# Optimization experiments

Measured on AMD Instinct MI355X. Metric: run time of the kernel, lower is better.

Reference implementation:

```python
import jax, jax.numpy as jnp
import numpy as np
import math

S, B, H, NH = 2048, 2, 2048, 16
HN = H // NH  # 128, head dim


def _rope_cache(seq_len, hn):
    # inv_freqs over even indices, half_hn entries
    inv_freqs = 0.0001 ** (jnp.arange(0, hn, 2, dtype=jnp.float32) / hn)
    pos = jnp.arange(seq_len, dtype=jnp.float32)
    angles = pos[:, None] * inv_freqs  # [s, hn/2]
    return jnp.cos(angles), jnp.sin(angles)


def _apply_rope(x, cos, sin):
    # x: [s, b, np, hn]; cos/sin: [s, hn/2] broadcast over b, np
    half = x.shape[-1] // 2
    c = cos[:, None, None, :]
    s = sin[:, None, None, :]
    left, right = x[..., :half], x[..., half:]
    return jnp.concatenate((c * left - s * right, s * left + c * right), axis=-1)


def setup_inputs() -> dict:
    key = jax.random.key(0)
    k0, k1, k2 = jax.random.split(key, 3)
    hidden_states = jax.random.normal(k0, (S, B, H), dtype=jnp.float32)
    # causal additive mask, broadcast over batch and heads
    causal = jnp.tril(jnp.ones((S, S), dtype=bool))
    attention_mask = jnp.where(causal, 0.0, -1e9).astype(jnp.float32)[None, None]
    W_qkv = jax.random.normal(k1, (3 * H, H), dtype=jnp.float32) * 0.02
    b_qkv = jnp.zeros((3 * H,), dtype=jnp.float32)
    W_dense = jax.random.normal(k2, (H, H), dtype=jnp.float32) * 0.02
    b_dense = jnp.zeros((H,), dtype=jnp.float32)
    return {"hidden_states": hidden_states, "attention_mask": attention_mask,
            "W_qkv": W_qkv, "b_qkv": b_qkv, "W_dense": W_dense, "b_dense": b_dense}


def reference(hidden_states, attention_mask, W_qkv, b_qkv, W_dense, b_dense):
    s, b, h = hidden_states.shape
    # fused QKV projection: [s,b,3h] -> [s,b,np,3*hn] -> split per head
    mixed = hidden_states @ W_qkv.T + b_qkv
    mixed = mixed.reshape(s, b, NH, 3 * HN)
    q, k, v = jnp.split(mixed, 3, axis=-1)  # each [s,b,np,hn]
    cos, sin = _rope_cache(s, HN)
    q = _apply_rope(q, cos, sin)
    k = _apply_rope(k, cos, sin)
    norm_factor = math.sqrt(HN)  # coeff is None (scale_attn_by_inverse_layer_idx=False)
    scores = jnp.einsum('sbnh,tbnh->bnst', q, k) / norm_factor  # [b,np,sq,sk]
    scores = scores + attention_mask
    probs = jax.nn.softmax(scores, axis=-1)  # dropout p=0 in eval
    ctx = jnp.einsum('bnst,tbnh->sbnh', probs, v).reshape(s, b, h)
    return ctx @ W_dense.T + b_dense  # [s,b,h]
```

## Files before the change

### kernel.cpp

```cpp
#include <hip/hip_runtime.h>

#define SEQ   2048
#define BATCH 2
#define HID   2048
#define NHEAD 16
#define HDIM  128
#define MTOT  4096
#define KDIM  2048

typedef __attribute__((ext_vector_type(8))) short  bf16x8;
typedef __attribute__((ext_vector_type(4))) float  f32x4;
typedef __attribute__((ext_vector_type(4))) unsigned short u16x4;
typedef __attribute__((ext_vector_type(8))) unsigned short u16x8;

__device__ __forceinline__ unsigned short f2bf(float x) {
  unsigned u = __float_as_uint(x);
  u += 0x7fffu + ((u >> 16) & 1u);
  return (unsigned short)(u >> 16);
}

__device__ __forceinline__ float fexp2(float x) {
  float r;
  asm("v_exp_f32 %0, %1" : "=v"(r) : "v"(x));
  return r;
}

__device__ __forceinline__ void gl_lds16(const void* g, void* l) {
  __builtin_amdgcn_global_load_lds(
      (__attribute__((address_space(1))) void*)g,
      (__attribute__((address_space(3))) void*)l, 16, 0, 0);
}

__device__ __forceinline__ f32x4 mfma16(bf16x8 a, bf16x8 b, f32x4 c) {
  return __builtin_amdgcn_mfma_f32_16x16x32_bf16(a, b, c, 0, 0, 0);
}

__global__ __launch_bounds__(256, 8)
void prep(const float* __restrict__ hidden, const float* __restrict__ Wqkv,
          const float* __restrict__ Wd,
          unsigned short* __restrict__ hidb, unsigned short* __restrict__ wqkvb,
          unsigned short* __restrict__ wdb,
          float* __restrict__ cosT, float* __restrict__ sinT) {
  int bid = blockIdx.x;
  if (bid < 24576) {
    const float* src; unsigned short* dst; int lb;
    if (bid < 8192)       { src = hidden; dst = hidb;  lb = bid; }
    else if (bid < 20480) { src = Wqkv;   dst = wqkvb; lb = bid - 8192; }
    else                  { src = Wd;     dst = wdb;   lb = bid - 20480; }
    int i = lb * 256 + threadIdx.x;
    int base = i << 2;
    int r = base >> 11, k = base & 2047;
    f32x4 v = *(const f32x4*)(src + base);
    int kp = k ^ (((r >> 1) & 7) << 3);
    u16x4 o;
    o[0] = f2bf(v[0]); o[1] = f2bf(v[1]); o[2] = f2bf(v[2]); o[3] = f2bf(v[3]);
    *(u16x4*)(dst + (size_t)r * 2048 + kp) = o;
  } else {
    int idx = (bid - 24576) * 256 + threadIdx.x;
    int s = idx >> 6, i = idx & 63;
    float inv = powf(1e-4f, (float)i * (1.0f / 64.0f));
    float a = (float)s * inv;
    cosT[idx] = cosf(a);
    sinT[idx] = sinf(a);
  }
}

__global__ __launch_bounds__(512, 2)
void gemm_qkv(const unsigned short* __restrict__ A,
              const unsigned short* __restrict__ Bt,
              const float* __restrict__ bias,
              unsigned short* __restrict__ Qs,
              unsigned short* __restrict__ Ks,
              unsigned short* __restrict__ Vt,
              const float* __restrict__ cosT,
              const float* __restrict__ sinT)
{
  __shared__ alignas(16) char lds[147456];
  const int tid = threadIdx.x;
  const int wid = tid >> 6, lane = tid & 63, g = lane >> 4, c = lane & 15;
  const int wr = wid >> 2, wc = wid & 3;

  const int bid = blockIdx.x;
  const int swz = (bid & 7) * 64 + (bid >> 3);
  const int nblk = swz & 15, mblk = swz >> 4;
  const int m0 = mblk << 7;
  const int n0 = nblk * 384;
  const int nh = nblk;

  char* ldsb = (char*)lds;
  const int sw = c >> 1;
  const char* ldsA0 = ldsb + (wr * 64 + c) * 128 + ((g ^ sw) << 4);
  const char* ldsA1 = ldsb + (wr * 64 + c) * 128 + (((4 + g) ^ sw) << 4);
  const char* ldsB0 = ldsb + 49152 + (wc * 16 + c) * 128 + ((g ^ sw) << 4);
  const char* ldsB1 = ldsb + 49152 + (wc * 16 + c) * 128 + (((4 + g) ^ sw) << 4);

  const char* gA = (const char*)A  + (size_t)(m0 + (tid >> 3)) * 4096 + (tid & 7) * 16;
  const char* gB = (const char*)Bt + (size_t)(n0 + (tid >> 3)) * 4096 + (tid & 7) * 16;
  char* lA = ldsb + tid * 16;
  char* lB = ldsb + 49152 + tid * 16;

#define STG_A(T, BUF) do { const char* _g = gA + (T) * 128; char* _l = lA + (BUF) * 16384; \
    gl_lds16(_g, _l); gl_lds16(_g + 262144, _l + 8192); } while (0)
#define STG_B(T, BUF) do { const char* _g = gB + (T) * 128; char* _l = lB + (BUF) * 49152; \
    gl_lds16(_g, _l);           gl_lds16(_g + 262144, _l + 8192);   \
    gl_lds16(_g + 524288, _l + 16384); gl_lds16(_g + 786432, _l + 24576); \
    gl_lds16(_g + 1048576, _l + 32768); gl_lds16(_g + 1310720, _l + 40960); } while (0)

  f32x4 acc[4][6];
#pragma unroll
  for (int i = 0; i < 4; ++i)
#pragma unroll
    for (int j = 0; j < 6; ++j) {
      acc[i][j][0] = 0.f; acc[i][j][1] = 0.f; acc[i][j][2] = 0.f; acc[i][j][3] = 0.f;
    }

  bf16x8 a[4], b[6];
  const int NT = KDIM / 64;

#define HALF(PA, PB, SA, SB) do {                                           \
    _Pragma("unroll")                                                       \
    for (int mf = 0; mf < 4; ++mf)                                          \
      a[mf] = *(const bf16x8*)(PA + (SA) * 16384 + mf * 2048);              \
    _Pragma("unroll")                                                       \
    for (int nl = 0; nl < 6; ++nl)                                          \
      b[nl] = *(const bf16x8*)(PB + (SB) * 49152 + nl * 8192);              \
    __builtin_amdgcn_s_setprio(1);                                          \
    _Pragma("unroll")                                                       \
    for (int mf = 0; mf < 4; ++mf)                                          \
      _Pragma("unroll")                                                     \
      for (int nl = 0; nl < 6; ++nl)                                        \
        acc[mf][nl] = mfma16(a[mf], b[nl], acc[mf][nl]);                    \
    __builtin_amdgcn_s_setprio(0);                                          \
  } while (0)

#define TILE(T, SA, SB) do {                                                \
    if ((T) + 1 < NT) { STG_B((T) + 1, ((T) + 1) & 1); }                    \
    if ((T) + 2 < NT) { STG_A((T) + 2, ((T) + 2) % 3); }                    \
    HALF(ldsA0, ldsB0, SA, SB);                                             \
    HALF(ldsA1, ldsB1, SA, SB);                                             \
    if ((T) + 2 < NT) { asm volatile("s_waitcnt vmcnt(2)" ::: "memory"); }  \
    else              { asm volatile("s_waitcnt vmcnt(0)" ::: "memory"); }  \
    __builtin_amdgcn_s_barrier();                                           \
  } while (0)

  STG_B(0, 0); STG_A(0, 0); STG_A(1, 1);
  asm volatile("s_waitcnt vmcnt(2)" ::: "memory");
  __builtin_amdgcn_s_barrier();

  for (int t = 0; t < 30; t += 6) {
    TILE(t + 0, 0, 0);
    TILE(t + 1, 1, 1);
    TILE(t + 2, 2, 0);
    TILE(t + 3, 0, 1);
    TILE(t + 4, 1, 0);
    TILE(t + 5, 2, 1);
  }
  TILE(30, 0, 0);
  TILE(31, 1, 1);

  const float qsc = 0.08838834764831845f * 1.4426950408889634f;
  const int dl = wc * 16 + c;
  unsigned short* Vtmp = (unsigned short*)ldsb;
  const int s0 = m0 >> 1;
#pragma unroll
  for (int ar = 0; ar < 4; ++ar) {
#pragma unroll
    for (int rr = 0; rr < 4; ++rr) {
      int m = m0 + wr * 64 + ar * 16 + g * 4 + rr;
      int s = m >> 1, bb = m & 1;
      size_t plane = (size_t)(bb * NHEAD + nh) * (SEQ * HDIM);
      int swb = (s & 7) << 3;
      float co = cosT[s * 64 + dl], si = sinT[s * 64 + dl];
      {
        float xl = acc[ar][0][rr] + bias[n0 + dl];
        float xr = acc[ar][1][rr] + bias[n0 + 64 + dl];
        Qs[plane + (size_t)s * HDIM + (dl ^ swb)]        = f2bf((co * xl - si * xr) * qsc);
        Qs[plane + (size_t)s * HDIM + ((dl + 64) ^ swb)] = f2bf((si * xl + co * xr) * qsc);
      }
      {
        float xl = acc[ar][2][rr] + bias[n0 + 128 + dl];
        float xr = acc[ar][3][rr] + bias[n0 + 192 + dl];
        Ks[plane + (size_t)s * HDIM + (dl ^ swb)]        = f2bf(co * xl - si * xr);
        Ks[plane + (size_t)s * HDIM + ((dl + 64) ^ swb)] = f2bf(si * xl + co * xr);
      }
      {
        int sloc = s - s0;
        Vtmp[(bb * 64 + sloc) * 136 + dl]      = f2bf(acc[ar][4][rr] + bias[n0 + 256 + dl]);
        Vtmp[(bb * 64 + sloc) * 136 + dl + 64] = f2bf(acc[ar][5][rr] + bias[n0 + 320 + dl]);
      }
    }
  }
  __syncthreads();
  {
    int b2 = tid >> 8, r = tid & 255;
    int d = r >> 1, half = r & 1;
    size_t planeV = (size_t)(b2 * NHEAD + nh) * (SEQ * HDIM);
    unsigned short* dstp = Vt + planeV + (size_t)d * SEQ + s0;
    int swb = (d & 7) << 3;
#pragma unroll
    for (int gg = 0; gg < 4; ++gg) {
      u16x8 v;
#pragma unroll
      for (int e = 0; e < 8; ++e)
        v[e] = Vtmp[(b2 * 64 + half * 32 + gg * 8 + e) * 136 + d];
      int tloc = half * 32 + gg * 8;
      *(u16x8*)(dstp + (tloc ^ swb)) = v;
    }
  }
#undef TILE
#undef HALF
#undef STG_A
#undef STG_B
}

__global__ __launch_bounds__(512, 2)
void gemm_out(const unsigned short* __restrict__ A,
              const unsigned short* __restrict__ Bt,
              const float* __restrict__ bias,
              float* __restrict__ Cout)
{
  __shared__ alignas(16) char lds[147456];
  const int tid = threadIdx.x;
  const int wid = tid >> 6, lane = tid & 63, g = lane >> 4, c = lane & 15;
  const int wr = wid >> 2, wc = wid & 3;

  const int bid = blockIdx.x;
  const int swz = (bid & 7) * 32 + (bid >> 3);
  const int nblk = swz >> 5, mblk = swz & 31;
  const int m0 = mblk << 7, n0 = nblk << 8;

  char* ldsb = (char*)lds;
  const int sw = c >> 1;
  const char* ldsA0 = ldsb + (wr * 64 + c) * 128 + ((g ^ sw) << 4);
  const char* ldsA1 = ldsb + (wr * 64 + c) * 128 + (((4 + g) ^ sw) << 4);
  const char* ldsB0 = ldsb + 49152 + (wc * 64 + c) * 128 + ((g ^ sw) << 4);
  const char* ldsB1 = ldsb + 49152 + (wc * 64 + c) * 128 + (((4 + g) ^ sw) << 4);

  const char* gA = (const char*)A  + (size_t)(m0 + (tid >> 3)) * 4096 + (tid & 7) * 16;
  const char* gB = (const char*)Bt + (size_t)(n0 + (tid >> 3)) * 4096 + (tid & 7) * 16;
  char* lA = ldsb + tid * 16;
  char* lB = ldsb + 49152 + tid * 16;

#define STG_A(T, BUF) do { const char* _g = gA + (T) * 128; char* _l = lA + (BUF) * 16384; \
    gl_lds16(_g, _l); gl_lds16(_g + 262144, _l + 8192); } while (0)
#define STG_B(T, BUF) do { const char* _g = gB + (T) * 128; char* _l = lB + (BUF) * 32768; \
    gl_lds16(_g, _l);           gl_lds16(_g + 262144, _l + 8192);   \
    gl_lds16(_g + 524288, _l + 16384); gl_lds16(_g + 786432, _l + 24576); } while (0)

  f32x4 acc[4][4];
#pragma unroll
  for (int i = 0; i < 4; ++i)
#pragma unroll
    for (int j = 0; j < 4; ++j) {
      acc[i][j][0] = 0.f; acc[i][j][1] = 0.f; acc[i][j][2] = 0.f; acc[i][j][3] = 0.f;
    }

  bf16x8 a[4], b[4];
  const int NT = KDIM / 64;

#define HALF(PA, PB, S) do {                                                \
    _Pragma("unroll")                                                       \
    for (int mf = 0; mf < 4; ++mf)                                          \
      a[mf] = *(const bf16x8*)(PA + (S) * 16384 + mf * 2048);               \
    _Pragma("unroll")                                                       \
    for (int nl = 0; nl < 4; ++nl)                                          \
      b[nl] = *(const bf16x8*)(PB + (S) * 32768 + nl * 2048);               \
    __builtin_amdgcn_s_setprio(1);                                          \
    _Pragma("unroll")                                                       \
    for (int mf = 0; mf < 4; ++mf)                                          \
      _Pragma("unroll")                                                     \
      for (int nl = 0; nl < 4; ++nl)                                        \
        acc[mf][nl] = mfma16(a[mf], b[nl], acc[mf][nl]);                    \
    __builtin_amdgcn_s_setprio(0);                                          \
  } while (0)

#define TILE(T, S) do {                                                     \
    if ((T) + 2 < NT) { STG_B((T) + 2, ((T) + 2) % 3); STG_A((T) + 2, ((T) + 2) % 3); } \
    HALF(ldsA0, ldsB0, S);                                                  \
    HALF(ldsA1, ldsB1, S);                                                  \
    if ((T) + 2 < NT) { asm volatile("s_waitcnt vmcnt(6)" ::: "memory"); }  \
    else              { asm volatile("s_waitcnt vmcnt(0)" ::: "memory"); }  \
    __builtin_amdgcn_s_barrier();                                           \
  } while (0)

  STG_B(0, 0); STG_A(0, 0);
  STG_B(1, 1); STG_A(1, 1);
  asm volatile("s_waitcnt vmcnt(6)" ::: "memory");
  __builtin_amdgcn_s_barrier();

  for (int t = 0; t < 30; t += 3) {
    TILE(t, 0);
    TILE(t + 1, 1);
    TILE(t + 2, 2);
  }
  TILE(30, 0);
  TILE(31, 1);

#pragma unroll
  for (int mf = 0; mf < 4; ++mf)
#pragma unroll
    for (int rr = 0; rr < 4; ++rr) {
      int m = m0 + wr * 64 + mf * 16 + g * 4 + rr;
#pragma unroll
      for (int nl = 0; nl < 4; ++nl) {
        int n = n0 + wc * 64 + nl * 16 + c;
        Cout[(size_t)m * HID + n] = acc[mf][nl][rr] + bias[n];
      }
    }
#undef TILE
#undef HALF
#undef STG_A
#undef STG_B
}

__global__ __launch_bounds__(512, 2)
void attn(const unsigned short* __restrict__ Qs,
          const unsigned short* __restrict__ Ks,
          const unsigned short* __restrict__ Vt,
          unsigned short* __restrict__ ctx)
{
  __shared__ alignas(16) unsigned short Klds[2][64 * 128];
  __shared__ alignas(16) unsigned short Vlds[128 * 64];
  __shared__ alignas(16) unsigned short Plds[256 * 72];
  const int tid = threadIdx.x;
  const int w = tid >> 6, lane = tid & 63, g = lane >> 4, c = lane & 15;
  const int bid = blockIdx.x;
  const int head = bid & 31;
  const int j = bid >> 5;
  const int qbh = 15 - j;
  const int q0w = (w < 4) ? ((qbh << 7) + w * 32) : ((j << 7) + (w - 4) * 32);
  const size_t plane = (size_t)head * (SEQ * HDIM);
  const unsigned short* Qp = Qs + plane;

  bf16x8 qf[2][4];
#pragma unroll
  for (int q2 = 0; q2 < 2; ++q2) {
    int s = q0w + q2 * 16 + c;
    int swb = (s & 7) << 3;
#pragma unroll
    for (int kk = 0; kk < 4; ++kk) {
      int d0 = kk * 32 + g * 8;
      qf[q2][kk] = *(const bf16x8*)(Qp + (size_t)s * HDIM + (d0 ^ swb));
    }
  }

  f32x4 accO[2][8];
#pragma unroll
  for (int i = 0; i < 2; ++i)
#pragma unroll
    for (int jj = 0; jj < 8; ++jj) {
      accO[i][jj][0] = 0.f; accO[i][jj][1] = 0.f; accO[i][jj][2] = 0.f; accO[i][jj][3] = 0.f;
    }
  float mrun[2] = { -1e30f, -1e30f };
  float lrun[2] = { 0.f, 0.f };

  const char* Kg = (const char*)(Ks + plane) + (tid >> 4) * 256 + (tid & 15) * 16;
  const char* Vg = (const char*)(Vt + plane) + (size_t)(tid >> 3) * 4096 + (tid & 7) * 16;

  const int ntiles = (qbh << 1) + 2;
  const int qminw = q0w;
  const int qmaxw = q0w + 31;

  gl_lds16(Kg,        (char*)Klds[0] + tid * 16);
  gl_lds16(Kg + 8192, (char*)Klds[0] + tid * 16 + 8192);

  for (int kt = 0; kt < ntiles; ++kt) {
    const int t0 = kt << 6;
    const bool havenext = (kt + 1 < ntiles);

    gl_lds16(Vg + t0 * 2,          (char*)Vlds + tid * 16);
    gl_lds16(Vg + t0 * 2 + 262144, (char*)Vlds + tid * 16 + 8192);
    if (havenext) {
      char* kd = (char*)Klds[(kt + 1) & 1] + tid * 16;
      gl_lds16(Kg + (size_t)(t0 + 64) * 256,        kd);
      gl_lds16(Kg + (size_t)(t0 + 64) * 256 + 8192, kd + 8192);
    }
    if (havenext) asm volatile("s_waitcnt vmcnt(4)" ::: "memory");
    else          asm volatile("s_waitcnt vmcnt(2)" ::: "memory");
    __builtin_amdgcn_s_barrier();

    if (t0 <= qmaxw) {
      const char* Kb = (const char*)Klds[kt & 1];
      f32x4 sacc[4][2];
#pragma unroll
      for (int i = 0; i < 4; ++i)
#pragma unroll
        for (int jj = 0; jj < 2; ++jj) {
          sacc[i][jj][0] = 0.f; sacc[i][jj][1] = 0.f; sacc[i][jj][2] = 0.f; sacc[i][jj][3] = 0.f;
        }
      __builtin_amdgcn_s_setprio(1);
#pragma unroll
      for (int kk = 0; kk < 4; ++kk) {
        bf16x8 kf[4];
#pragma unroll
        for (int ta = 0; ta < 4; ++ta) {
          int t = ta * 16 + c;
          int d0 = kk * 32 + g * 8;
          kf[ta] = *(const bf16x8*)(Kb + t * 256 + ((d0 ^ ((t & 7) << 3)) << 1));
        }
#pragma unroll
        for (int ta = 0; ta < 4; ++ta)
#pragma unroll
          for (int q2 = 0; q2 < 2; ++q2)
            sacc[ta][q2] = mfma16(kf[ta], qf[q2][kk], sacc[ta][q2]);
      }
      __builtin_amdgcn_s_setprio(0);

      if (t0 + 63 > qminw) {
#pragma unroll
        for (int ta = 0; ta < 4; ++ta)
#pragma unroll
          for (int q2 = 0; q2 < 2; ++q2)
#pragma unroll
            for (int r = 0; r < 4; ++r) {
              int t = t0 + ta * 16 + g * 4 + r;
              int q = qminw + q2 * 16 + c;
              if (t > q) sacc[ta][q2][r] = -30000.f;
            }
      }

      float corr[2];
      bool resc = false;
#pragma unroll
      for (int q2 = 0; q2 < 2; ++q2) {
        float mx = -30000.f;
#pragma unroll
        for (int ta = 0; ta < 4; ++ta)
          mx = fmaxf(mx, fmaxf(fmaxf(sacc[ta][q2][0], sacc[ta][q2][1]),
                               fmaxf(sacc[ta][q2][2], sacc[ta][q2][3])));
        mx = fmaxf(mx, __shfl_xor(mx, 16));
        mx = fmaxf(mx, __shfl_xor(mx, 32));
        bool rs = mx > mrun[q2] + 8.0f;
        resc |= rs;
        float mnew = rs ? mx : mrun[q2];
        corr[q2] = fexp2(mrun[q2] - mnew);
        mrun[q2] = mnew;
        float ls = 0.f;
#pragma unroll
        for (int ta = 0; ta < 4; ++ta)
#pragma unroll
          for (int r = 0; r < 4; ++r) {
            float e = fexp2(sacc[ta][q2][r] - mnew);
            sacc[ta][q2][r] = e;
            ls += e;
          }
        ls += __shfl_xor(ls, 16);
        ls += __shfl_xor(ls, 32);
        lrun[q2] = lrun[q2] * corr[q2] + ls;
      }

      if (__any(resc)) {
#pragma unroll
        for (int q2 = 0; q2 < 2; ++q2)
#pragma unroll
          for (int r = 0; r < 4; ++r) {
            float cD = __shfl(corr[q2], (lane & 48) | (((lane >> 4) << 2) + r));
#pragma unroll
            for (int fn = 0; fn < 8; ++fn) accO[q2][fn][r] *= cD;
          }
      }

#pragma unroll
      for (int q2 = 0; q2 < 2; ++q2) {
        int prow = w * 32 + q2 * 16 + c;
#pragma unroll
        for (int ta = 0; ta < 4; ++ta) {
          u16x4 pk;
          pk[0] = f2bf(sacc[ta][q2][0]); pk[1] = f2bf(sacc[ta][q2][1]);
          pk[2] = f2bf(sacc[ta][q2][2]); pk[3] = f2bf(sacc[ta][q2][3]);
          *(u16x4*)(&Plds[prow * 72 + ta * 16 + g * 4]) = pk;
        }
      }
    }

    if (havenext) asm volatile("s_waitcnt vmcnt(2)" ::: "memory");
    else          asm volatile("s_waitcnt vmcnt(0)" ::: "memory");
    __builtin_amdgcn_s_barrier();

    if (t0 <= qmaxw) {
      __builtin_amdgcn_s_setprio(1);
#pragma unroll
      for (int kk = 0; kk < 2; ++kk) {
        bf16x8 pa[2];
#pragma unroll
        for (int q2 = 0; q2 < 2; ++q2)
          pa[q2] = *(const bf16x8*)((const char*)Plds + (w * 32 + q2 * 16 + c) * 144 + (kk * 32 + g * 8) * 2);
#pragma unroll
        for (int fn = 0; fn < 8; ++fn) {
          int d = fn * 16 + c;
          int tt = kk * 32 + g * 8;
          bf16x8 vb = *(const bf16x8*)((const char*)Vlds + d * 128 + ((tt ^ ((d & 7) << 3)) << 1));
#pragma unroll
          for (int q2 = 0; q2 < 2; ++q2)
            accO[q2][fn] = mfma16(pa[q2], vb, accO[q2][fn]);
        }
      }
      __builtin_amdgcn_s_setprio(0);
    }
    __builtin_amdgcn_s_barrier();
  }

  const int b = head >> 4, nh = head & 15;
  float linv[2] = { 1.0f / lrun[0], 1.0f / lrun[1] };
#pragma unroll
  for (int q2 = 0; q2 < 2; ++q2)
#pragma unroll
    for (int r = 0; r < 4; ++r) {
      float inv = __shfl(linv[q2], (lane & 48) | (((lane >> 4) << 2) + r));
      int q = q0w + q2 * 16 + g * 4 + r;
      int m = q * 2 + b;
      int swb = ((m >> 1) & 7) << 3;
#pragma unroll
      for (int fn = 0; fn < 8; ++fn) {
        int h = nh * 128 + fn * 16 + c;
        ctx[(size_t)m * HID + (h ^ swb)] = f2bf(accO[q2][fn][r] * inv);
      }
    }
}

extern "C" void kernel_launch(void* const* d_in, const int* in_sizes, int n_in,
                              void* d_out, int out_size, void* d_ws, size_t ws_size,
                              hipStream_t stream) {
  const float* hidden = (const float*)d_in[0];
  const float* Wqkv = (const float*)d_in[2];
  const float* bqkv = (const float*)d_in[3];
  const float* Wd   = (const float*)d_in[4];
  const float* bd   = (const float*)d_in[5];
  float* out = (float*)d_out;
  char* ws = (char*)d_ws;

  const size_t OFF_HID  = 0;
  const size_t OFF_WQKV = 16777216;
  const size_t OFF_WD   = 41943040;
  const size_t OFF_COS  = 50331648;
  const size_t OFF_SIN  = 50855936;
  const size_t OFF_Q    = 51380224;
  const size_t OFF_K    = 68157440;
  const size_t OFF_VT   = 84934656;
  if (ws_size < 101711872) return;

  unsigned short* hidb  = (unsigned short*)(ws + OFF_HID);
  unsigned short* wqkvb = (unsigned short*)(ws + OFF_WQKV);
  unsigned short* wdb   = (unsigned short*)(ws + OFF_WD);
  float* cosT = (float*)(ws + OFF_COS);
  float* sinT = (float*)(ws + OFF_SIN);
  unsigned short* Qsb = (unsigned short*)(ws + OFF_Q);
  unsigned short* Ksb = (unsigned short*)(ws + OFF_K);
  unsigned short* Vtb = (unsigned short*)(ws + OFF_VT);
  unsigned short* ctxb = hidb;

  prep<<<25088, 256, 0, stream>>>(hidden, Wqkv, Wd, hidb, wqkvb, wdb, cosT, sinT);

  gemm_qkv<<<512, 512, 0, stream>>>(hidb, wqkvb, bqkv, Qsb, Ksb, Vtb, cosT, sinT);
  attn<<<256, 512, 0, stream>>>(Qsb, Ksb, Vtb, ctxb);
  gemm_out<<<256, 512, 0, stream>>>(ctxb, wdb, bd, out);
}
```

Measured before the change: 231.3 us.

## Triple-buffer K/V tiles in attention and drop the mid-iteration barrier

The attention loop now keeps three LDS buffers each for K and V and prefetches both tiles two iterations ahead, instead of double-buffering K and loading V inside the iteration. The barrier between the softmax P write and the PV MFMAs is replaced by a per-wave lgkmcnt wait, since each wave only reads its own P rows. This leaves one block-wide barrier per tile and gives global loads more time to complete. The cost is more LDS per block (about 132KB), which may limit occupancy, and tighter reliance on correct vmcnt accounting.

After: 236.2 us. 1.02x slower.

```diff
diff --git a/kernel.cpp b/kernel.cpp
--- a/kernel.cpp
+++ b/kernel.cpp
@@ -319,8 +319,8 @@
           const unsigned short* __restrict__ Vt,
           unsigned short* __restrict__ ctx)
 {
-  __shared__ alignas(16) unsigned short Klds[2][64 * 128];
-  __shared__ alignas(16) unsigned short Vlds[128 * 64];
+  __shared__ alignas(16) unsigned short Klds[3][64 * 128];
+  __shared__ alignas(16) unsigned short Vlds[3][64 * 128];
   __shared__ alignas(16) unsigned short Plds[256 * 72];
   const int tid = threadIdx.x;
   const int w = tid >> 6, lane = tid & 63, g = lane >> 4, c = lane & 15;
@@ -361,26 +361,28 @@
   const int qminw = q0w;
   const int qmaxw = q0w + 31;
 
-  gl_lds16(Kg,        (char*)Klds[0] + tid * 16);
-  gl_lds16(Kg + 8192, (char*)Klds[0] + tid * 16 + 8192);
+#define STG_KV(T) do {                                                      \
+    char* kd = (char*)Klds[(T) % 3] + tid * 16;                             \
+    gl_lds16(Kg + (size_t)(T) * 16384,        kd);                          \
+    gl_lds16(Kg + (size_t)(T) * 16384 + 8192, kd + 8192);                   \
+    char* vd = (char*)Vlds[(T) % 3] + tid * 16;                             \
+    gl_lds16(Vg + (T) * 128,          vd);                                  \
+    gl_lds16(Vg + (T) * 128 + 262144, vd + 8192);                           \
+  } while (0)
+
+  STG_KV(0);
+  STG_KV(1);
 
   for (int kt = 0; kt < ntiles; ++kt) {
     const int t0 = kt << 6;
-    const bool havenext = (kt + 1 < ntiles);
-
-    gl_lds16(Vg + t0 * 2,          (char*)Vlds + tid * 16);
-    gl_lds16(Vg + t0 * 2 + 262144, (char*)Vlds + tid * 16 + 8192);
-    if (havenext) {
-      char* kd = (char*)Klds[(kt + 1) & 1] + tid * 16;
-      gl_lds16(Kg + (size_t)(t0 + 64) * 256,        kd);
-      gl_lds16(Kg + (size_t)(t0 + 64) * 256 + 8192, kd + 8192);
-    }
-    if (havenext) asm volatile("s_waitcnt vmcnt(4)" ::: "memory");
-    else          asm volatile("s_waitcnt vmcnt(2)" ::: "memory");
+    if (kt + 1 < ntiles) asm volatile("s_waitcnt vmcnt(4)" ::: "memory");
+    else                 asm volatile("s_waitcnt vmcnt(0)" ::: "memory");
     __builtin_amdgcn_s_barrier();
+    if (kt + 2 < ntiles) STG_KV(kt + 2);
 
     if (t0 <= qmaxw) {
-      const char* Kb = (const char*)Klds[kt & 1];
+      const char* Kb = (const char*)Klds[kt % 3];
+      const char* Vb = (const char*)Vlds[kt % 3];
       f32x4 sacc[4][2];
 #pragma unroll
       for (int i = 0; i < 4; ++i)
@@ -471,13 +473,9 @@
           *(u16x4*)(&Plds[prow * 72 + ta * 16 + g * 4]) = pk;
         }
       }
-    }
-
-    if (havenext) asm volatile("s_waitcnt vmcnt(2)" ::: "memory");
-    else          asm volatile("s_waitcnt vmcnt(0)" ::: "memory");
-    __builtin_amdgcn_s_barrier();
-
-    if (t0 <= qmaxw) {
+      asm volatile("s_waitcnt lgkmcnt(0)" ::: "memory");
+      __builtin_amdgcn_sched_barrier(0);
+
       __builtin_amdgcn_s_setprio(1);
 #pragma unroll
       for (int kk = 0; kk < 2; ++kk) {
@@ -489,7 +487,7 @@
         for (int fn = 0; fn < 8; ++fn) {
           int d = fn * 16 + c;
           int tt = kk * 32 + g * 8;
-          bf16x8 vb = *(const bf16x8*)((const char*)Vlds + d * 128 + ((tt ^ ((d & 7) << 3)) << 1));
+          bf16x8 vb = *(const bf16x8*)(Vb + d * 128 + ((tt ^ ((d & 7) << 3)) << 1));
 #pragma unroll
           for (int q2 = 0; q2 < 2; ++q2)
             accO[q2][fn] = mfma16(pa[q2], vb, accO[q2][fn]);
@@ -497,8 +495,8 @@
       }
       __builtin_amdgcn_s_setprio(0);
     }
-    __builtin_amdgcn_s_barrier();
-  }
+  }
+#undef STG_KV
 
   const int b = head >> 4, nh = head & 15;
   float linv[2] = { 1.0f / lrun[0], 1.0f / lrun[1] };
```

## Split GEMM main loops into barrier-separated phases interleaving LDS reads, staging and MFMA

Applied to the files above, without the earlier changes.

Restructures the K loop of both the QKV GEMM and the output GEMM into several phases. Each phase issues LDS fragment reads plus a slice of the global-to-LDS staging, waits on lgkmcnt, then runs a block of MFMAs behind a sched_barrier. The aim is to spread global loads and LDS reads evenly across the MFMA work and keep waves in lockstep, a ping-pong style schedule. In exchange it adds extra workgroup barriers per tile and forbids the compiler from reordering across the phase boundaries.

Result: no change. 234.3 us (+1.3%).

```diff
diff --git a/kernel.cpp b/kernel.cpp
--- a/kernel.cpp
+++ b/kernel.cpp
@@ -101,10 +101,10 @@
 
 #define STG_A(T, BUF) do { const char* _g = gA + (T) * 128; char* _l = lA + (BUF) * 16384; \
     gl_lds16(_g, _l); gl_lds16(_g + 262144, _l + 8192); } while (0)
-#define STG_B(T, BUF) do { const char* _g = gB + (T) * 128; char* _l = lB + (BUF) * 49152; \
-    gl_lds16(_g, _l);           gl_lds16(_g + 262144, _l + 8192);   \
-    gl_lds16(_g + 524288, _l + 16384); gl_lds16(_g + 786432, _l + 24576); \
-    gl_lds16(_g + 1048576, _l + 32768); gl_lds16(_g + 1310720, _l + 40960); } while (0)
+#define STG_B2(T, BUF, I) do { const char* _g = gB + (T) * 128 + (I) * 524288; \
+    char* _l = lB + (BUF) * 49152 + (I) * 16384;                               \
+    gl_lds16(_g, _l); gl_lds16(_g + 262144, _l + 8192); } while (0)
+#define STG_B(T, BUF) do { STG_B2(T, BUF, 0); STG_B2(T, BUF, 1); STG_B2(T, BUF, 2); } while (0)
 
   f32x4 acc[4][6];
 #pragma unroll
@@ -114,33 +114,49 @@
       acc[i][j][0] = 0.f; acc[i][j][1] = 0.f; acc[i][j][2] = 0.f; acc[i][j][3] = 0.f;
     }
 
-  bf16x8 a[4], b[6];
+  bf16x8 a0[4], a1[4], bA[3], bB[3];
   const int NT = KDIM / 64;
 
-#define HALF(PA, PB, SA, SB) do {                                           \
-    _Pragma("unroll")                                                       \
+#define RD_A(AR, PTR, SA) do { _Pragma("unroll")                            \
     for (int mf = 0; mf < 4; ++mf)                                          \
-      a[mf] = *(const bf16x8*)(PA + (SA) * 16384 + mf * 2048);              \
-    _Pragma("unroll")                                                       \
-    for (int nl = 0; nl < 6; ++nl)                                          \
-      b[nl] = *(const bf16x8*)(PB + (SB) * 49152 + nl * 8192);              \
-    __builtin_amdgcn_s_setprio(1);                                          \
-    _Pragma("unroll")                                                       \
+      AR[mf] = *(const bf16x8*)(PTR + (SA) * 16384 + mf * 2048); } while (0)
+#define RD_B(BR, PTR, SB, NLO) do { _Pragma("unroll")                       \
+    for (int nl = 0; nl < 3; ++nl)                                          \
+      BR[nl] = *(const bf16x8*)(PTR + (SB) * 49152 + ((NLO) + nl) * 8192); } while (0)
+
+#define MF12(AR, BR, NLO) do { _Pragma("unroll")                            \
     for (int mf = 0; mf < 4; ++mf)                                          \
       _Pragma("unroll")                                                     \
-      for (int nl = 0; nl < 6; ++nl)                                        \
-        acc[mf][nl] = mfma16(a[mf], b[nl], acc[mf][nl]);                    \
+      for (int nl = 0; nl < 3; ++nl)                                        \
+        acc[mf][(NLO) + nl] = mfma16(AR[mf], BR[nl], acc[mf][(NLO) + nl]); } while (0)
+
+#define PH(READS, STAGE, MFMAS, VMW) do {                                   \
+    READS; STAGE;                                                           \
+    __builtin_amdgcn_s_barrier();                                           \
+    asm volatile("s_waitcnt lgkmcnt(0)" ::: "memory");                      \
+    __builtin_amdgcn_sched_barrier(0);                                      \
+    __builtin_amdgcn_s_setprio(1);                                          \
+    MFMAS;                                                                  \
     __builtin_amdgcn_s_setprio(0);                                          \
+    VMW;                                                                    \
+    __builtin_amdgcn_s_barrier();                                           \
   } while (0)
 
-#define TILE(T, SA, SB) do {                                                \
-    if ((T) + 1 < NT) { STG_B((T) + 1, ((T) + 1) & 1); }                    \
-    if ((T) + 2 < NT) { STG_A((T) + 2, ((T) + 2) % 3); }                    \
-    HALF(ldsA0, ldsB0, SA, SB);                                             \
-    HALF(ldsA1, ldsB1, SA, SB);                                             \
-    if ((T) + 2 < NT) { asm volatile("s_waitcnt vmcnt(2)" ::: "memory"); }  \
-    else              { asm volatile("s_waitcnt vmcnt(0)" ::: "memory"); }  \
-    __builtin_amdgcn_s_barrier();                                           \
+#define TILE(T, SA, SB) do {                                                          \
+    PH({ RD_A(a0, ldsA0, SA); RD_B(bA, ldsB0, SB, 0); },                              \
+       { if ((T) + 1 < NT) STG_B2((T) + 1, ((T) + 1) & 1, 0); },                      \
+       MF12(a0, bA, 0), ((void)0));                                                   \
+    PH({ RD_B(bB, ldsB0, SB, 3); },                                                   \
+       { if ((T) + 1 < NT) STG_B2((T) + 1, ((T) + 1) & 1, 1); },                      \
+       MF12(a0, bB, 3), ((void)0));                                                   \
+    PH({ RD_A(a1, ldsA1, SA); RD_B(bA, ldsB1, SB, 0); },                              \
+       { if ((T) + 1 < NT) STG_B2((T) + 1, ((T) + 1) & 1, 2); },                      \
+       MF12(a1, bA, 0), ((void)0));                                                   \
+    PH({ RD_B(bB, ldsB1, SB, 3); },                                                   \
+       { if ((T) + 2 < NT) STG_A((T) + 2, ((T) + 2) % 3); },                          \
+       MF12(a1, bB, 3),                                                               \
+       { if ((T) + 2 < NT) { asm volatile("s_waitcnt vmcnt(2)" ::: "memory"); }       \
+         else              { asm volatile("s_waitcnt vmcnt(0)" ::: "memory"); } });   \
   } while (0)
 
   STG_B(0, 0); STG_A(0, 0); STG_A(1, 1);
@@ -208,9 +224,13 @@
     }
   }
 #undef TILE
-#undef HALF
+#undef PH
+#undef MF12
+#undef RD_A
+#undef RD_B
 #undef STG_A
 #undef STG_B
+#undef STG_B2
 }
 
 __global__ __launch_bounds__(512, 2)
@@ -243,9 +263,9 @@
 
 #define STG_A(T, BUF) do { const char* _g = gA + (T) * 128; char* _l = lA + (BUF) * 16384; \
     gl_lds16(_g, _l); gl_lds16(_g + 262144, _l + 8192); } while (0)
-#define STG_B(T, BUF) do { const char* _g = gB + (T) * 128; char* _l = lB + (BUF) * 32768; \
-    gl_lds16(_g, _l);           gl_lds16(_g + 262144, _l + 8192);   \
-    gl_lds16(_g + 524288, _l + 16384); gl_lds16(_g + 786432, _l + 24576); } while (0)
+#define STG_B2(T, BUF, I) do { const char* _g = gB + (T) * 128 + (I) * 524288; \
+    char* _l = lB + (BUF) * 32768 + (I) * 16384;                               \
+    gl_lds16(_g, _l); gl_lds16(_g + 262144, _l + 8192); } while (0)
 
   f32x4 acc[4][4];
 #pragma unroll
@@ -255,36 +275,48 @@
       acc[i][j][0] = 0.f; acc[i][j][1] = 0.f; acc[i][j][2] = 0.f; acc[i][j][3] = 0.f;
     }
 
-  bf16x8 a[4], b[4];
+  bf16x8 a0[4], a1[4], b0[4], b1[4];
   const int NT = KDIM / 64;
 
-#define HALF(PA, PB, S) do {                                                \
-    _Pragma("unroll")                                                       \
+#define RD8(AR, BR, PA, PB, S) do { _Pragma("unroll")                       \
     for (int mf = 0; mf < 4; ++mf)                                          \
-      a[mf] = *(const bf16x8*)(PA + (S) * 16384 + mf * 2048);               \
+      AR[mf] = *(const bf16x8*)(PA + (S) * 16384 + mf * 2048);              \
     _Pragma("unroll")                                                       \
     for (int nl = 0; nl < 4; ++nl)                                          \
-      b[nl] = *(const bf16x8*)(PB + (S) * 32768 + nl * 2048);               \
-    __builtin_amdgcn_s_setprio(1);                                          \
-    _Pragma("unroll")                                                       \
+      BR[nl] = *(const bf16x8*)(PB + (S) * 32768 + nl * 2048); } while (0)
+
+#define MF16(AR, BR) do { _Pragma("unroll")                                 \
     for (int mf = 0; mf < 4; ++mf)                                          \
       _Pragma("unroll")                                                     \
       for (int nl = 0; nl < 4; ++nl)                                        \
-        acc[mf][nl] = mfma16(a[mf], b[nl], acc[mf][nl]);                    \
+        acc[mf][nl] = mfma16(AR[mf], BR[nl], acc[mf][nl]); } while (0)
+
+#define PH(READS, STAGE, MFMAS, VMW) do {                                   \
+    READS; STAGE;                                                           \
+    __builtin_amdgcn_s_barrier();                                           \
+    asm volatile("s_waitcnt lgkmcnt(0)" ::: "memory");                      \
+    __builtin_amdgcn_sched_barrier(0);                                      \
+    __builtin_amdgcn_s_setprio(1);                                          \
+    MFMAS;                                                                  \
     __builtin_amdgcn_s_setprio(0);                                          \
-  } while (0)
-
-#define TILE(T, S) do {                                                     \
-    if ((T) + 2 < NT) { STG_B((T) + 2, ((T) + 2) % 3); STG_A((T) + 2, ((T) + 2) % 3); } \
-    HALF(ldsA0, ldsB0, S);                                                  \
-    HALF(ldsA1, ldsB1, S);                                                  \
-    if ((T) + 2 < NT) { asm volatile("s_waitcnt vmcnt(6)" ::: "memory"); }  \
-    else              { asm volatile("s_waitcnt vmcnt(0)" ::: "memory"); }  \
+    VMW;                                                                    \
     __builtin_amdgcn_s_barrier();                                           \
   } while (0)
 
-  STG_B(0, 0); STG_A(0, 0);
-  STG_B(1, 1); STG_A(1, 1);
+#define TILE(T, S) do {                                                               \
+    PH(RD8(a0, b0, ldsA0, ldsB0, S),                                                  \
+       { if ((T) + 2 < NT) { STG_B2((T) + 2, ((T) + 2) % 3, 0);                       \
+                             STG_B2((T) + 2, ((T) + 2) % 3, 1); } },                  \
+       MF16(a0, b0), ((void)0));                                                      \
+    PH(RD8(a1, b1, ldsA1, ldsB1, S),                                                  \
+       { if ((T) + 2 < NT) STG_A((T) + 2, ((T) + 2) % 3); },                          \
+       MF16(a1, b1),                                                                  \
+       { if ((T) + 2 < NT) { asm volatile("s_waitcnt vmcnt(6)" ::: "memory"); }       \
+         else              { asm volatile("s_waitcnt vmcnt(0)" ::: "memory"); } });   \
+  } while (0)
+
+  STG_B2(0, 0, 0); STG_B2(0, 0, 1); STG_A(0, 0);
+  STG_B2(1, 1, 0); STG_B2(1, 1, 1); STG_A(1, 1);
   asm volatile("s_waitcnt vmcnt(6)" ::: "memory");
   __builtin_amdgcn_s_barrier();
 
@@ -308,9 +340,11 @@
       }
     }
 #undef TILE
-#undef HALF
+#undef PH
+#undef MF16
+#undef RD8
 #undef STG_A
-#undef STG_B
+#undef STG_B2
 }
 
 __global__ __launch_bounds__(512, 2)
```
